# Kernel tuning notes

Measured on AMD Instinct MI355X. Metric: run time of the kernel, lower is better.

The kernel has to match this reference:

```python
import jax, jax.numpy as jnp
import numpy as np

B, N, D_IN, D_OUT, H, ALPHA = 8, 2048, 128, 64, 1, 0.2


def setup_inputs() -> dict:
    key = jax.random.key(0)
    k1, k2, k3, k4 = jax.random.split(key, 4)
    x = jax.random.normal(k1, (B, N, D_IN), dtype=jnp.float32)
    adj = jax.random.randint(k2, (B, N, N), 0, 2, dtype=jnp.int32)
    # guarantee self-loops so no softmax row is entirely masked
    adj = jnp.maximum(adj, jnp.eye(N, dtype=jnp.int32)[None])
    # xavier_uniform with gain=1.414, as in the torch module
    lim_w = 1.414 * np.sqrt(6.0 / (D_IN + D_OUT * H))
    W = jax.random.uniform(k3, (D_OUT * H, D_IN), minval=-lim_w, maxval=lim_w, dtype=jnp.float32)
    b = jnp.zeros((D_OUT * H,), dtype=jnp.float32)
    lim_a = 1.414 * np.sqrt(6.0 / (H + 2 * D_OUT))
    a = jax.random.uniform(k4, (H, 2 * D_OUT), minval=-lim_a, maxval=lim_a, dtype=jnp.float32)
    return {"x": x, "adj_hat": adj, "W": W, "b": b, "a": a}


def reference(x, adj_hat, W, b, a):
    Bn, Nn = x.shape[:2]
    # projection: [B,N,d_in] -> [B,N,H,D]
    xp = (x @ W.T + b).reshape(Bn, Nn, H, D_OUT)
    # additive score a . [x_i ; x_j] split into two O(N) dot-products
    # (mathematically identical to the original O(N^2) concat formulation)
    a_src, a_dst = a[:, :D_OUT], a[:, D_OUT:]
    e_src = jnp.einsum('bnhd,hd->bnh', xp, a_src)  # score contribution of node i (query/p axis)
    e_dst = jnp.einsum('bnhd,hd->bnh', xp, a_dst)  # score contribution of node j (neighbor/q axis)
    e = e_src[:, :, None, :] + e_dst[:, None, :, :]  # [B,N,N,H]
    e = jax.nn.leaky_relu(e, ALPHA)
    e = jnp.where(adj_hat[..., None] == 0, -jnp.inf, e)
    att = jax.nn.softmax(e, axis=2)  # softmax over neighbor axis (torch dim=-2)
    res = jnp.einsum('bmnh,bnhd->bmhd', att, xp)  # weighted aggregation
    return res.reshape(Bn, Nn, H * D_OUT)  # concat_heads=True
```

## Files before the change

### kernel.cpp

```cpp
#include <hip/hip_runtime.h>
#include <hip/hip_bf16.h>
#include <cstdint>

#define NN 2048
#define BB 8
#define DIN 128
#define DOUT 64

typedef __attribute__((ext_vector_type(8))) short bf16x8;
typedef __attribute__((ext_vector_type(4))) float f32x4;

static __device__ __forceinline__ short f2b(float f) {
    union { __hip_bfloat16 h; short s; } u;
    u.h = __float2bfloat16(f);
    return u.s;
}

__global__ __launch_bounds__(256) void gat_xp_mfma(
    const float* __restrict__ x, const float* __restrict__ W,
    const float* __restrict__ bias, const float* __restrict__ a,
    unsigned short* __restrict__ xpT, float* __restrict__ e_src,
    float* __restrict__ e_dst)
{
    const int t = threadIdx.x;
    const int lane = t & 63;
    const int w = t >> 6;
    const int lr = lane & 15;
    const int g  = lane >> 4;
    const int r0 = blockIdx.x * 64 + w * 16;

    f32x4 acc[4] = {};
    const float* xrow = x + (size_t)(r0 + lr) * DIN + g * 8;
    #pragma unroll
    for (int ks = 0; ks < 4; ++ks) {
        const float4 xa = *(const float4*)(xrow + ks * 32);
        const float4 xb = *(const float4*)(xrow + ks * 32 + 4);
        bf16x8 afr;
        afr[0] = f2b(xa.x); afr[1] = f2b(xa.y); afr[2] = f2b(xa.z); afr[3] = f2b(xa.w);
        afr[4] = f2b(xb.x); afr[5] = f2b(xb.y); afr[6] = f2b(xb.z); afr[7] = f2b(xb.w);
        #pragma unroll
        for (int dt = 0; dt < 4; ++dt) {
            const float* wrow = W + (size_t)(dt * 16 + lr) * DIN + ks * 32 + g * 8;
            const float4 wa = *(const float4*)(wrow);
            const float4 wb = *(const float4*)(wrow + 4);
            bf16x8 bfr;
            bfr[0] = f2b(wa.x); bfr[1] = f2b(wa.y); bfr[2] = f2b(wa.z); bfr[3] = f2b(wa.w);
            bfr[4] = f2b(wb.x); bfr[5] = f2b(wb.y); bfr[6] = f2b(wb.z); bfr[7] = f2b(wb.w);
            acc[dt] = __builtin_amdgcn_mfma_f32_16x16x32_bf16(afr, bfr, acc[dt], 0, 0, 0);
        }
    }

    const int b  = r0 >> 11;
    const int nb = r0 & (NN - 1);
    float es[4] = {0.f, 0.f, 0.f, 0.f};
    float ed[4] = {0.f, 0.f, 0.f, 0.f};
    #pragma unroll
    for (int dt = 0; dt < 4; ++dt) {
        const int d = dt * 16 + lr;
        const float bv  = bias[d];
        const float asv = a[d];
        const float adv = a[DOUT + d];
        #pragma unroll
        for (int reg = 0; reg < 4; ++reg) {
            const float v = acc[dt][reg] + bv;
            const int n = nb + g * 4 + reg;
            xpT[((size_t)(b * DOUT + d) << 11) + n] = (unsigned short)f2b(v);
            es[reg] += v * asv;
            ed[reg] += v * adv;
        }
    }
    #pragma unroll
    for (int reg = 0; reg < 4; ++reg) {
        #pragma unroll
        for (int off = 1; off < 16; off <<= 1) {
            es[reg] += __shfl_xor(es[reg], off);
            ed[reg] += __shfl_xor(ed[reg], off);
        }
    }
    if (lr == 0) {
        #pragma unroll
        for (int reg = 0; reg < 4; ++reg) {
            e_src[r0 + g * 4 + reg] = es[reg];
            e_dst[r0 + g * 4 + reg] = ed[reg];
        }
    }
}

__global__ __launch_bounds__(256) void gat_dmax(
    const float* __restrict__ e_dst, float* __restrict__ dmax)
{
    __shared__ float red[4];
    const int b = blockIdx.x, t = threadIdx.x;
    float m = -1e30f;
    #pragma unroll
    for (int i = 0; i < 8; ++i)
        m = fmaxf(m, e_dst[(size_t)b * NN + i * 256 + t]);
    #pragma unroll
    for (int off = 32; off >= 1; off >>= 1)
        m = fmaxf(m, __shfl_xor(m, off));
    if ((t & 63) == 0) red[t >> 6] = m;
    __syncthreads();
    if (t == 0) dmax[b] = fmaxf(fmaxf(red[0], red[1]), fmaxf(red[2], red[3]));
}

__global__ __launch_bounds__(256) void gat_attn_mfma(
    const int* __restrict__ adj, const unsigned short* __restrict__ xpT,
    const float* __restrict__ e_src, const float* __restrict__ e_dst,
    const float* __restrict__ dmax, float* __restrict__ out)
{
    __shared__ float d_lds[NN];
    __shared__ float o_lds[4 * 16 * 65];
    __shared__ float rs_lds[4 * 16];

    const int t = threadIdx.x;
    const int lane = t & 63;
    const int w = t >> 6;
    const int lr = lane & 15;
    const int g  = lane >> 4;
    const int b  = blockIdx.x >> 7;
    const int m0 = (blockIdx.x & 127) * 16;
    const size_t base = (size_t)b * NN;

    #pragma unroll
    for (int i = 0; i < 8; ++i)
        d_lds[i * 256 + t] = e_dst[base + i * 256 + t];
    __syncthreads();

    const float s_r = e_src[base + m0 + lr];
    const float e0  = s_r + dmax[b];
    const float bnd = fmaxf(e0, 0.2f * e0);

    const int n_base = w * 512;
    const int* __restrict__ adjrow = adj + ((base + m0 + lr) << 11);
    const unsigned short* __restrict__ xb = xpT + ((size_t)(b * DOUT) << 11);

    f32x4 acc[4] = {};
    float rs = 0.f;

    for (int ks = 0; ks < 16; ++ks) {
        const int n0 = n_base + ks * 32 + g * 8;
        const int4   a0 = *(const int4*)(adjrow + n0);
        const int4   a1 = *(const int4*)(adjrow + n0 + 4);
        const float4 d0 = *(const float4*)(d_lds + n0);
        const float4 d1 = *(const float4*)(d_lds + n0 + 4);
        const float dv[8] = {d0.x, d0.y, d0.z, d0.w, d1.x, d1.y, d1.z, d1.w};
        const int   av[8] = {a0.x, a0.y, a0.z, a0.w, a1.x, a1.y, a1.z, a1.w};
        float pv[8];
        #pragma unroll
        for (int j = 0; j < 8; ++j) {
            const float e = s_r + dv[j];
            const float le = fmaxf(e, 0.2f * e);
            const float pe = __expf(le - bnd);
            pv[j] = av[j] ? pe : 0.f;
            rs += pv[j];
        }
        bf16x8 afr;
        #pragma unroll
        for (int j = 0; j < 8; ++j) afr[j] = f2b(pv[j]);
        #pragma unroll
        for (int dt = 0; dt < 4; ++dt) {
            const bf16x8 bfr = *(const bf16x8*)(xb + ((size_t)(dt * 16 + lr) << 11) + n0);
            acc[dt] = __builtin_amdgcn_mfma_f32_16x16x32_bf16(afr, bfr, acc[dt], 0, 0, 0);
        }
    }

    rs += __shfl_xor(rs, 16);
    rs += __shfl_xor(rs, 32);
    if (lane < 16) rs_lds[w * 16 + lane] = rs;

    #pragma unroll
    for (int dt = 0; dt < 4; ++dt)
        #pragma unroll
        for (int reg = 0; reg < 4; ++reg)
            o_lds[w * 1040 + (g * 4 + reg) * 65 + dt * 16 + lr] = acc[dt][reg];
    __syncthreads();

    #pragma unroll
    for (int i = 0; i < 4; ++i) {
        const int idx = i * 256 + t;
        const int row = idx >> 6;
        const int d   = idx & 63;
        const float v = o_lds[row * 65 + d] + o_lds[1040 + row * 65 + d]
                      + o_lds[2080 + row * 65 + d] + o_lds[3120 + row * 65 + d];
        const float rst = rs_lds[row] + rs_lds[16 + row]
                        + rs_lds[32 + row] + rs_lds[48 + row];
        out[(base + m0 + row) * DOUT + d] = v / rst;
    }
}

extern "C" void kernel_launch(void* const* d_in, const int* in_sizes, int n_in,
                              void* d_out, int out_size, void* d_ws, size_t ws_size,
                              hipStream_t stream) {
    const float* x    = (const float*)d_in[0];
    const int*   adj  = (const int*)d_in[1];
    const float* W    = (const float*)d_in[2];
    const float* bvec = (const float*)d_in[3];
    const float* a    = (const float*)d_in[4];
    float* out = (float*)d_out;

    unsigned short* xpT = (unsigned short*)d_ws;
    float* e_src = (float*)((char*)d_ws + (1 << 21));
    float* e_dst = e_src + (size_t)BB * NN;
    float* dmax  = e_dst + (size_t)BB * NN;

    gat_xp_mfma<<<256, 256, 0, stream>>>(x, W, bvec, a, xpT, e_src, e_dst);
    gat_dmax<<<BB, 256, 0, stream>>>(e_dst, dmax);
    gat_attn_mfma<<<BB * 128, 256, 0, stream>>>(adj, xpT, e_src, e_dst, dmax, out);
}
```

Baseline: 226.3 us.

## Restructure attention: coalesced adj rows, LDS-staged probabilities, per-wave output columns

The attention kernel now reads adjacency rows fully coalesced, with each wave loading contiguous 256-column chunks of four rows and prefetching the next phase into registers. It stages the bf16 probabilities through a double-buffered LDS tile so that each wave computes a disjoint 16-column slice of the output, which removes the cross-wave output reduction. The separate dmax kernel is folded into the attention prologue, and the projection kernel splits K across waves with an LDS reduction over smaller blocks. The cost is a barrier per phase and redundant per-block max computation.

```diff
diff --git a/kernel.cpp b/kernel.cpp
--- a/kernel.cpp
+++ b/kernel.cpp
@@ -6,12 +6,15 @@
 #define BB 8
 #define DIN 128
 #define DOUT 64
+#define PHN 256
+#define NPH (NN / PHN)
+#define PCH 130
 
 typedef __attribute__((ext_vector_type(8))) short bf16x8;
 typedef __attribute__((ext_vector_type(4))) float f32x4;
 
-static __device__ __forceinline__ short f2b(float f) {
-    union { __hip_bfloat16 h; short s; } u;
+static __device__ __forceinline__ unsigned short f2b(float f) {
+    union { __hip_bfloat16 h; unsigned short s; } u;
     u.h = __float2bfloat16(f);
     return u.s;
 }
@@ -22,95 +25,74 @@
     unsigned short* __restrict__ xpT, float* __restrict__ e_src,
     float* __restrict__ e_dst)
 {
+    __shared__ float red[4 * 16 * 65];
     const int t = threadIdx.x;
     const int lane = t & 63;
     const int w = t >> 6;
     const int lr = lane & 15;
     const int g  = lane >> 4;
-    const int r0 = blockIdx.x * 64 + w * 16;
-
-    f32x4 acc[4] = {};
-    const float* xrow = x + (size_t)(r0 + lr) * DIN + g * 8;
-    #pragma unroll
-    for (int ks = 0; ks < 4; ++ks) {
-        const float4 xa = *(const float4*)(xrow + ks * 32);
-        const float4 xb = *(const float4*)(xrow + ks * 32 + 4);
-        bf16x8 afr;
-        afr[0] = f2b(xa.x); afr[1] = f2b(xa.y); afr[2] = f2b(xa.z); afr[3] = f2b(xa.w);
-        afr[4] = f2b(xb.x); afr[5] = f2b(xb.y); afr[6] = f2b(xb.z); afr[7] = f2b(xb.w);
-        #pragma unroll
-        for (int dt = 0; dt < 4; ++dt) {
-            const float* wrow = W + (size_t)(dt * 16 + lr) * DIN + ks * 32 + g * 8;
-            const float4 wa = *(const float4*)(wrow);
-            const float4 wb = *(const float4*)(wrow + 4);
-            bf16x8 bfr;
-            bfr[0] = f2b(wa.x); bfr[1] = f2b(wa.y); bfr[2] = f2b(wa.z); bfr[3] = f2b(wa.w);
-            bfr[4] = f2b(wb.x); bfr[5] = f2b(wb.y); bfr[6] = f2b(wb.z); bfr[7] = f2b(wb.w);
-            acc[dt] = __builtin_amdgcn_mfma_f32_16x16x32_bf16(afr, bfr, acc[dt], 0, 0, 0);
-        }
-    }
-
-    const int b  = r0 >> 11;
-    const int nb = r0 & (NN - 1);
-    float es[4] = {0.f, 0.f, 0.f, 0.f};
-    float ed[4] = {0.f, 0.f, 0.f, 0.f};
+    const int r0 = blockIdx.x * 16;
+    const int k0 = w * 32 + g * 8;
+
+    const float* xr = x + (size_t)(r0 + lr) * DIN + k0;
+    const float4 xa = *(const float4*)xr;
+    const float4 xb4 = *(const float4*)(xr + 4);
+    bf16x8 afr;
+    afr[0]=f2b(xa.x);  afr[1]=f2b(xa.y);  afr[2]=f2b(xa.z);  afr[3]=f2b(xa.w);
+    afr[4]=f2b(xb4.x); afr[5]=f2b(xb4.y); afr[6]=f2b(xb4.z); afr[7]=f2b(xb4.w);
+
     #pragma unroll
     for (int dt = 0; dt < 4; ++dt) {
-        const int d = dt * 16 + lr;
-        const float bv  = bias[d];
-        const float asv = a[d];
-        const float adv = a[DOUT + d];
-        #pragma unroll
-        for (int reg = 0; reg < 4; ++reg) {
-            const float v = acc[dt][reg] + bv;
-            const int n = nb + g * 4 + reg;
-            xpT[((size_t)(b * DOUT + d) << 11) + n] = (unsigned short)f2b(v);
-            es[reg] += v * asv;
-            ed[reg] += v * adv;
-        }
-    }
-    #pragma unroll
-    for (int reg = 0; reg < 4; ++reg) {
-        #pragma unroll
-        for (int off = 1; off < 16; off <<= 1) {
-            es[reg] += __shfl_xor(es[reg], off);
-            ed[reg] += __shfl_xor(ed[reg], off);
-        }
-    }
-    if (lr == 0) {
-        #pragma unroll
-        for (int reg = 0; reg < 4; ++reg) {
-            e_src[r0 + g * 4 + reg] = es[reg];
-            e_dst[r0 + g * 4 + reg] = ed[reg];
-        }
-    }
-}
-
-__global__ __launch_bounds__(256) void gat_dmax(
-    const float* __restrict__ e_dst, float* __restrict__ dmax)
-{
-    __shared__ float red[4];
-    const int b = blockIdx.x, t = threadIdx.x;
-    float m = -1e30f;
-    #pragma unroll
-    for (int i = 0; i < 8; ++i)
-        m = fmaxf(m, e_dst[(size_t)b * NN + i * 256 + t]);
-    #pragma unroll
-    for (int off = 32; off >= 1; off >>= 1)
-        m = fmaxf(m, __shfl_xor(m, off));
-    if ((t & 63) == 0) red[t >> 6] = m;
-    __syncthreads();
-    if (t == 0) dmax[b] = fmaxf(fmaxf(red[0], red[1]), fmaxf(red[2], red[3]));
+        const float* wr = W + (size_t)(dt * 16 + lr) * DIN + k0;
+        const float4 wa = *(const float4*)wr;
+        const float4 wb = *(const float4*)(wr + 4);
+        bf16x8 bfr;
+        bfr[0]=f2b(wa.x); bfr[1]=f2b(wa.y); bfr[2]=f2b(wa.z); bfr[3]=f2b(wa.w);
+        bfr[4]=f2b(wb.x); bfr[5]=f2b(wb.y); bfr[6]=f2b(wb.z); bfr[7]=f2b(wb.w);
+        f32x4 acc = {0.f, 0.f, 0.f, 0.f};
+        acc = __builtin_amdgcn_mfma_f32_16x16x32_bf16(afr, bfr, acc, 0, 0, 0);
+        #pragma unroll
+        for (int reg = 0; reg < 4; ++reg)
+            red[w * 1040 + (g * 4 + reg) * 65 + dt * 16 + lr] = acc[reg];
+    }
+    __syncthreads();
+
+    const int row = t >> 4;
+    const int dq  = t & 15;
+    const int b   = r0 >> 11;
+    const int nb  = r0 & (NN - 1);
+    float es = 0.f, ed = 0.f;
+    #pragma unroll
+    for (int j = 0; j < 4; ++j) {
+        const int d = dq * 4 + j;
+        const float v = red[0 * 1040 + row * 65 + d] + red[1 * 1040 + row * 65 + d]
+                      + red[2 * 1040 + row * 65 + d] + red[3 * 1040 + row * 65 + d]
+                      + bias[d];
+        es += v * a[d];
+        ed += v * a[DOUT + d];
+        xpT[((size_t)(b * DOUT + d) << 11) + nb + row] = f2b(v);
+    }
+    es += __shfl_xor(es, 1); es += __shfl_xor(es, 2);
+    es += __shfl_xor(es, 4); es += __shfl_xor(es, 8);
+    ed += __shfl_xor(ed, 1); ed += __shfl_xor(ed, 2);
+    ed += __shfl_xor(ed, 4); ed += __shfl_xor(ed, 8);
+    if (dq == 0) {
+        e_src[r0 + row] = es;
+        e_dst[r0 + row] = ed;
+    }
 }
 
 __global__ __launch_bounds__(256) void gat_attn_mfma(
     const int* __restrict__ adj, const unsigned short* __restrict__ xpT,
     const float* __restrict__ e_src, const float* __restrict__ e_dst,
-    const float* __restrict__ dmax, float* __restrict__ out)
+    float* __restrict__ out)
 {
     __shared__ float d_lds[NN];
-    __shared__ float o_lds[4 * 16 * 65];
-    __shared__ float rs_lds[4 * 16];
+    __shared__ unsigned short p_lds[2][32 * PCH];
+    __shared__ float mred[4];
+    __shared__ float s_lds[16];
+    __shared__ float bnd_lds[16];
+    __shared__ float rs_lds[16];
 
     const int t = threadIdx.x;
     const int lane = t & 63;
@@ -121,70 +103,110 @@
     const int m0 = (blockIdx.x & 127) * 16;
     const size_t base = (size_t)b * NN;
 
-    #pragma unroll
-    for (int i = 0; i < 8; ++i)
-        d_lds[i * 256 + t] = e_dst[base + i * 256 + t];
-    __syncthreads();
-
-    const float s_r = e_src[base + m0 + lr];
-    const float e0  = s_r + dmax[b];
-    const float bnd = fmaxf(e0, 0.2f * e0);
-
-    const int n_base = w * 512;
-    const int* __restrict__ adjrow = adj + ((base + m0 + lr) << 11);
-    const unsigned short* __restrict__ xb = xpT + ((size_t)(b * DOUT) << 11);
-
-    f32x4 acc[4] = {};
-    float rs = 0.f;
-
-    for (int ks = 0; ks < 16; ++ks) {
-        const int n0 = n_base + ks * 32 + g * 8;
-        const int4   a0 = *(const int4*)(adjrow + n0);
-        const int4   a1 = *(const int4*)(adjrow + n0 + 4);
-        const float4 d0 = *(const float4*)(d_lds + n0);
-        const float4 d1 = *(const float4*)(d_lds + n0 + 4);
-        const float dv[8] = {d0.x, d0.y, d0.z, d0.w, d1.x, d1.y, d1.z, d1.w};
-        const int   av[8] = {a0.x, a0.y, a0.z, a0.w, a1.x, a1.y, a1.z, a1.w};
-        float pv[8];
-        #pragma unroll
-        for (int j = 0; j < 8; ++j) {
-            const float e = s_r + dv[j];
-            const float le = fmaxf(e, 0.2f * e);
-            const float pe = __expf(le - bnd);
-            pv[j] = av[j] ? pe : 0.f;
-            rs += pv[j];
+    float dm = -1e30f;
+    #pragma unroll
+    for (int i = 0; i < 8; ++i) {
+        const float v = e_dst[base + i * 256 + t];
+        d_lds[i * 256 + t] = v;
+        dm = fmaxf(dm, v);
+    }
+    #pragma unroll
+    for (int off = 32; off >= 1; off >>= 1) dm = fmaxf(dm, __shfl_xor(dm, off));
+    if (lane == 0) mred[w] = dm;
+    __syncthreads();
+    const float dmax = fmaxf(fmaxf(mred[0], mred[1]), fmaxf(mred[2], mred[3]));
+    if (t < 16) {
+        const float s = e_src[base + m0 + t];
+        const float e0 = s + dmax;
+        s_lds[t] = s;
+        bnd_lds[t] = fmaxf(e0, 0.2f * e0);
+    }
+    __syncthreads();
+
+    float srow[4], brow[4];
+    const int* aptr[4];
+    #pragma unroll
+    for (int it = 0; it < 4; ++it) {
+        const int row = it * 4 + w;
+        srow[it] = s_lds[row];
+        brow[it] = bnd_lds[row];
+        aptr[it] = adj + ((base + (size_t)(m0 + row)) << 11) + lane * 4;
+    }
+
+    int4 acur[4], anxt[4];
+    #pragma unroll
+    for (int it = 0; it < 4; ++it) acur[it] = *(const int4*)(aptr[it]);
+
+    f32x4 acc = {0.f, 0.f, 0.f, 0.f};
+    float rs_acc[4] = {0.f, 0.f, 0.f, 0.f};
+    const unsigned short* xb = xpT + ((size_t)(b * DOUT + w * 16 + lr) << 11);
+
+    const int c  = lane >> 1;
+    const int jj = (lane & 1) * 4;
+
+    int buf = 0;
+    for (int ph = 0; ph < NPH; ++ph) {
+        if (ph + 1 < NPH) {
+            #pragma unroll
+            for (int it = 0; it < 4; ++it)
+                anxt[it] = *(const int4*)(aptr[it] + (ph + 1) * PHN);
         }
-        bf16x8 afr;
-        #pragma unroll
-        for (int j = 0; j < 8; ++j) afr[j] = f2b(pv[j]);
-        #pragma unroll
-        for (int dt = 0; dt < 4; ++dt) {
-            const bf16x8 bfr = *(const bf16x8*)(xb + ((size_t)(dt * 16 + lr) << 11) + n0);
-            acc[dt] = __builtin_amdgcn_mfma_f32_16x16x32_bf16(afr, bfr, acc[dt], 0, 0, 0);
+        const float4 dv = *(const float4*)(d_lds + ph * PHN + lane * 4);
+        const float dvv[4] = {dv.x, dv.y, dv.z, dv.w};
+        unsigned short* pb = &p_lds[buf][0];
+        #pragma unroll
+        for (int it = 0; it < 4; ++it) {
+            const int row = it * 4 + w;
+            const float s = srow[it], bd = brow[it];
+            const int av[4] = {acur[it].x, acur[it].y, acur[it].z, acur[it].w};
+            float p[4];
+            #pragma unroll
+            for (int j = 0; j < 4; ++j) {
+                const float e = s + dvv[j];
+                const float le = fmaxf(e, 0.2f * e);
+                const float pe = __expf(le - bd);
+                p[j] = av[j] ? pe : 0.f;
+            }
+            rs_acc[it] += p[0] + p[1] + p[2] + p[3];
+            unsigned int* pp32 =
+                (unsigned int*)(pb + c * PCH + row * 8 + jj);
+            pp32[0] = ((unsigned)f2b(p[1]) << 16) | f2b(p[0]);
+            pp32[1] = ((unsigned)f2b(p[3]) << 16) | f2b(p[2]);
         }
-    }
-
-    rs += __shfl_xor(rs, 16);
-    rs += __shfl_xor(rs, 32);
-    if (lane < 16) rs_lds[w * 16 + lane] = rs;
-
-    #pragma unroll
-    for (int dt = 0; dt < 4; ++dt)
-        #pragma unroll
-        for (int reg = 0; reg < 4; ++reg)
-            o_lds[w * 1040 + (g * 4 + reg) * 65 + dt * 16 + lr] = acc[dt][reg];
-    __syncthreads();
-
-    #pragma unroll
-    for (int i = 0; i < 4; ++i) {
-        const int idx = i * 256 + t;
-        const int row = idx >> 6;
-        const int d   = idx & 63;
-        const float v = o_lds[row * 65 + d] + o_lds[1040 + row * 65 + d]
-                      + o_lds[2080 + row * 65 + d] + o_lds[3120 + row * 65 + d];
-        const float rst = rs_lds[row] + rs_lds[16 + row]
-                        + rs_lds[32 + row] + rs_lds[48 + row];
-        out[(base + m0 + row) * DOUT + d] = v / rst;
+        __syncthreads();
+        const unsigned int* pw = (const unsigned int*)pb;
+        const int nb0 = ph * PHN;
+        #pragma unroll
+        for (int ks = 0; ks < 8; ++ks) {
+            const int cc = ks * 4 + g;
+            const int wbase = cc * 65 + lr * 4;
+            union { unsigned int u[4]; bf16x8 v; } af;
+            af.u[0] = pw[wbase + 0];
+            af.u[1] = pw[wbase + 1];
+            af.u[2] = pw[wbase + 2];
+            af.u[3] = pw[wbase + 3];
+            const bf16x8 bfr = *(const bf16x8*)(xb + nb0 + ks * 32 + g * 8);
+            acc = __builtin_amdgcn_mfma_f32_16x16x32_bf16(af.v, bfr, acc, 0, 0, 0);
+        }
+        #pragma unroll
+        for (int it = 0; it < 4; ++it) acur[it] = anxt[it];
+        buf ^= 1;
+    }
+
+    #pragma unroll
+    for (int it = 0; it < 4; ++it) {
+        float v = rs_acc[it];
+        #pragma unroll
+        for (int off = 32; off >= 1; off >>= 1) v += __shfl_xor(v, off);
+        if (lane == 0) rs_lds[it * 4 + w] = v;
+    }
+    __syncthreads();
+
+    #pragma unroll
+    for (int reg = 0; reg < 4; ++reg) {
+        const int row = g * 4 + reg;
+        const float o = acc[reg] / rs_lds[row];
+        out[(base + (size_t)(m0 + row)) * DOUT + w * 16 + lr] = o;
     }
 }
 
@@ -201,9 +223,7 @@
     unsigned short* xpT = (unsigned short*)d_ws;
     float* e_src = (float*)((char*)d_ws + (1 << 21));
     float* e_dst = e_src + (size_t)BB * NN;
-    float* dmax  = e_dst + (size_t)BB * NN;
-
-    gat_xp_mfma<<<256, 256, 0, stream>>>(x, W, bvec, a, xpT, e_src, e_dst);
-    gat_dmax<<<BB, 256, 0, stream>>>(e_dst, dmax);
-    gat_attn_mfma<<<BB * 128, 256, 0, stream>>>(adj, xpT, e_src, e_dst, dmax, out);
-}
+
+    gat_xp_mfma<<<(BB * NN) / 16, 256, 0, stream>>>(x, W, bvec, a, xpT, e_src, e_dst);
+    gat_attn_mfma<<<BB * (NN / 16), 256, 0, stream>>>(adj, xpT, e_src, e_dst, out);
+}
```

Result: faster. 214.7 us (-5.1%).
